# Optimization experiments

Hardware: AMD Instinct MI355X
Metric: run time of the kernel (lower is better)

The kernel has to match this reference:

```python
import jax, jax.numpy as jnp
import numpy as np

N_SURF, N_GRAPH, K_EIG = 30000, 12000, 128
C_IN_SURF, C_IN_GRAPH, C_OUT = 5, 20, 1
HID = 64  # C_width // 2
N_BLOCK = 4
NEIGH_TH = 8.0
BOX = 90.0
E_GRAPH = 192000


def _build_bipartite(rng):
    # exact math of compute_bipartite_graphs: cdist < neigh_th, w = exp(-d/sigma)
    verts = rng.random((N_SURF, 3), dtype=np.float32) * BOX
    pos = rng.random((N_GRAPH, 3), dtype=np.float32) * BOX
    sigma = NEIGH_TH / 2.0
    srcs, dsts, ws = [], [], []
    pn = (pos * pos).sum(-1)
    for s in range(0, N_SURF, 2048):
        ch = verts[s:s + 2048]
        d2 = (ch * ch).sum(-1)[:, None] + pn[None, :] - 2.0 * ch @ pos.T
        d = np.sqrt(np.maximum(d2, 0.0))
        ii, jj = np.where(d < NEIGH_TH)
        srcs.append(ii + s)
        dsts.append(jj + N_SURF)  # graph nodes offset by n_surf
        ws.append(np.exp(-d[ii, jj] / sigma))
    return (np.concatenate(srcs).astype(np.int64),
            np.concatenate(dsts).astype(np.int64),
            np.concatenate(ws).astype(np.float32))


def setup_inputs() -> dict:
    key = jax.random.key(0)
    ks = iter(jax.random.split(key, 64))
    rng = np.random.default_rng(0)
    bi_surf, bi_graph, bi_w = _build_bipartite(rng)

    def rn(shape, scale=0.05):
        return jax.random.normal(next(ks), shape, jnp.float32) * scale

    inp = {
        'x_surf': rn((N_SURF, C_IN_SURF), 1.0),
        'x_graph': rn((N_GRAPH, C_IN_GRAPH), 1.0),
        'mass': jax.random.uniform(next(ks), (N_SURF,), jnp.float32) + 0.1,
        'evals': jnp.sort(jax.random.uniform(next(ks), (K_EIG,), jnp.float32)) * 100.0,
        'evecs': rn((N_SURF, K_EIG), 1.0) / np.sqrt(N_SURF),
        'bi_w': jnp.asarray(bi_w),
        'lin1_w': rn((C_IN_SURF, HID)), 'lin1_b': jnp.zeros((HID,), jnp.float32),
        'lin2_w': rn((C_IN_GRAPH, HID)), 'lin2_b': jnp.zeros((HID,), jnp.float32),
        'diff_time': jax.random.uniform(next(ks), (N_BLOCK, HID), jnp.float32) * 0.1 + 1e-3,
        'mlp_w0': rn((N_BLOCK, 2 * HID, HID)), 'mlp_b0': jnp.zeros((N_BLOCK, HID), jnp.float32),
        'mlp_w1': rn((N_BLOCK, HID, HID)), 'mlp_b1': jnp.zeros((N_BLOCK, HID), jnp.float32),
        'mlp_w2': rn((N_BLOCK, HID, HID)), 'mlp_b2': jnp.zeros((N_BLOCK, HID), jnp.float32),
        'gcn_w1': rn((N_BLOCK, HID, HID)), 'gcn_b1': jnp.zeros((N_BLOCK, HID), jnp.float32),
        'gcn_w2': rn((N_BLOCK, HID, HID)), 'gcn_b2': jnp.zeros((N_BLOCK, HID), jnp.float32),
        'gs_w': rn((N_BLOCK - 1, HID, HID)), 'gs_b': jnp.zeros((N_BLOCK - 1, HID), jnp.float32),
        'gs_w_last': rn((HID, C_OUT)), 'gs_b_last': jnp.zeros((C_OUT,), jnp.float32),
        'sg_w': rn((N_BLOCK - 1, HID, HID)), 'sg_b': jnp.zeros((N_BLOCK - 1, HID), jnp.float32),
        'sg_w_last': rn((HID, C_OUT)), 'sg_b_last': jnp.zeros((C_OUT,), jnp.float32),
        'graph_edge_index': jax.random.randint(next(ks), (2, E_GRAPH), 0, N_GRAPH, jnp.int64),
        'bi_surf': jnp.asarray(bi_surf),
        'bi_graph': jnp.asarray(bi_graph),
    }
    return inp


def gcn_conv(x, W, b, src, dst, ew, n):
    # PyG GCNConv: sym-normalized aggregation with self loops (weight 1)
    h = x @ W
    w = ew if ew is not None else jnp.ones(src.shape, x.dtype)
    deg = jnp.ones((n,), x.dtype).at[dst].add(w)
    dinv = jnp.where(deg > 0, jax.lax.rsqrt(deg), 0.0)
    norm = dinv[src] * dinv[dst] * w
    out = jnp.zeros((n, h.shape[1]), x.dtype).at[dst].add(norm[:, None] * h[src])
    return out + (dinv * dinv)[:, None] * h + b


def reference(x_surf, x_graph, mass, evals, evecs, bi_w,
              lin1_w, lin1_b, lin2_w, lin2_b,
              diff_time, mlp_w0, mlp_b0, mlp_w1, mlp_b1, mlp_w2, mlp_b2,
              gcn_w1, gcn_b1, gcn_w2, gcn_b2,
              gs_w, gs_b, gs_w_last, gs_b_last,
              sg_w, sg_b, sg_w_last, sg_b_last,
              graph_edge_index, bi_surf, bi_graph):
    n_surf, n_graph = x_surf.shape[0], x_graph.shape[0]
    n_tot = n_surf + n_graph
    diff_x = x_surf @ lin1_w + lin1_b            # [Ns, HID]
    g_x = x_graph @ lin2_w + lin2_b              # [Ng, HID]
    gsrc, gdst = graph_edge_index[0], graph_edge_index[1]

    for i in range(N_BLOCK):
        # --- DiffusionNet block (spectral diffusion + MLP + skip) ---
        t = jnp.clip(diff_time[i], 1e-8)
        x_spec = evecs.T @ (mass[:, None] * diff_x)                  # [K, HID]
        x_diffuse = evecs @ (jnp.exp(-evals[:, None] * t[None, :]) * x_spec)
        feat = jnp.concatenate([diff_x, x_diffuse], axis=-1)
        h = jax.nn.relu(feat @ mlp_w0[i] + mlp_b0[i])
        h = jax.nn.relu(h @ mlp_w1[i] + mlp_b1[i])
        h = h @ mlp_w2[i] + mlp_b2[i]
        diff_x = diff_x + h
        # --- internal GCN on molecular graph (use_distance=False) ---
        hg = jax.nn.relu(gcn_conv(g_x, gcn_w1[i], gcn_b1[i], gsrc, gdst, None, n_graph))
        g_x = gcn_conv(hg, gcn_w2[i], gcn_b2[i], gsrc, gdst, None, n_graph)
        # --- bipartite mixing over combined node set ---
        x_cat = jnp.concatenate([diff_x, g_x], axis=0)               # [Ns+Ng, HID]
        if i < N_BLOCK - 1:
            new_surf = gcn_conv(x_cat, gs_w[i], gs_b[i], bi_graph, bi_surf, bi_w, n_tot)[:n_surf]
            new_graph = gcn_conv(x_cat, sg_w[i], sg_b[i], bi_surf, bi_graph, bi_w, n_tot)[n_surf:]
        else:
            new_surf = gcn_conv(x_cat, gs_w_last, gs_b_last, bi_graph, bi_surf, bi_w, n_tot)[:n_surf]
            new_graph = gcn_conv(x_cat, sg_w_last, sg_b_last, bi_surf, bi_graph, bi_w, n_tot)[n_surf:]
        diff_x, g_x = new_surf, new_graph

    return jnp.concatenate([diff_x, g_x], axis=0)  # [Ns+Ng, C_out]
```

## Files before the change

kernel.cpp:

```cpp
#include <hip/hip_runtime.h>

#define N_SURF 30000
#define N_GRAPH 12000
#define K_EIG 128
#define HID 64
#define E_GRAPH 192000

static inline int cdiv(int a, int b) { return (a + b - 1) / b; }

__global__ void k_fill(float* __restrict__ p, float v, int n) {
    int t = blockIdx.x * blockDim.x + threadIdx.x;
    if (t < n) p[t] = v;
}

__global__ void k_filli(int* __restrict__ p, int v, int n) {
    int t = blockIdx.x * blockDim.x + threadIdx.x;
    if (t < n) p[t] = v;
}

__global__ void k_to_dinv(float* __restrict__ p, int n) {
    int t = blockIdx.x * blockDim.x + threadIdx.x;
    if (t < n) p[t] = 1.0f / sqrtf(p[t]);
}

__global__ void k_deg_graph(const int* __restrict__ gdst, float* __restrict__ deg, int E) {
    int t = blockIdx.x * blockDim.x + threadIdx.x;
    if (t < E) atomicAdd(&deg[gdst[t]], 1.0f);
}

__global__ void k_deg_bi(const int* __restrict__ bs, const int* __restrict__ bg,
                         const float* __restrict__ w, float* __restrict__ deg_s,
                         float* __restrict__ deg_g, int E) {
    int t = blockIdx.x * blockDim.x + threadIdx.x;
    if (t < E) {
        float wv = w[t];
        atomicAdd(&deg_s[bs[t]], wv);
        atomicAdd(&deg_g[bg[t] - N_SURF], wv);
    }
}

__global__ void k_hist_bi(const int* __restrict__ bs, const int* __restrict__ bg,
                          int* __restrict__ cnt_s, int* __restrict__ cnt_g, int E) {
    int t = blockIdx.x * blockDim.x + threadIdx.x;
    if (t < E) {
        atomicAdd(&cnt_s[bs[t]], 1);
        atomicAdd(&cnt_g[bg[t] - N_SURF], 1);
    }
}

__global__ void k_hist_gr(const int* __restrict__ gdst, int* __restrict__ cnt, int E) {
    int t = blockIdx.x * blockDim.x + threadIdx.x;
    if (t < E) atomicAdd(&cnt[gdst[t]], 1);
}

__global__ __launch_bounds__(256) void k_scan(const int* __restrict__ cnt,
                                              int* __restrict__ rowptr, int n) {
    __shared__ int part[256];
    int per = (n + 255) / 256;
    int lo = threadIdx.x * per, hi = min(lo + per, n);
    int s = 0;
    for (int i = lo; i < hi; ++i) s += cnt[i];
    part[threadIdx.x] = s;
    __syncthreads();
    for (int off = 1; off < 256; off <<= 1) {
        int v = (threadIdx.x >= off) ? part[threadIdx.x - off] : 0;
        __syncthreads();
        part[threadIdx.x] += v;
        __syncthreads();
    }
    int base = (threadIdx.x == 0) ? 0 : part[threadIdx.x - 1];
    for (int i = lo; i < hi; ++i) { rowptr[i] = base; base += cnt[i]; }
    if (threadIdx.x == 0) rowptr[n] = part[255];
}

__global__ void k_fill_csr_bi(const int* __restrict__ bs, const int* __restrict__ bg,
                              const float* __restrict__ w, const float* __restrict__ dinv_s,
                              const float* __restrict__ dinv_g,
                              const int* __restrict__ rp_s, int* __restrict__ cur_s,
                              int* __restrict__ csr_s_src, float* __restrict__ csr_s_nrm,
                              const int* __restrict__ rp_g, int* __restrict__ cur_g,
                              int* __restrict__ csr_g_src, float* __restrict__ csr_g_nrm,
                              int E) {
    int t = blockIdx.x * blockDim.x + threadIdx.x;
    if (t >= E) return;
    int s = bs[t], g = bg[t] - N_SURF;
    float wv = w[t];
    int ps = rp_s[s] + atomicAdd(&cur_s[s], 1);
    csr_s_src[ps] = g;
    csr_s_nrm[ps] = dinv_s[s] * wv;
    int pg = rp_g[g] + atomicAdd(&cur_g[g], 1);
    csr_g_src[pg] = s;
    csr_g_nrm[pg] = dinv_g[g] * wv;
}

__global__ void k_fill_csr_gr(const int* __restrict__ ei, const float* __restrict__ dinv,
                              const int* __restrict__ rp, int* __restrict__ cur,
                              int* __restrict__ csr_src, float* __restrict__ csr_nrm, int E) {
    int t = blockIdx.x * blockDim.x + threadIdx.x;
    if (t >= E) return;
    int s = ei[t], d = ei[E + t];
    int p = rp[d] + atomicAdd(&cur[d], 1);
    csr_src[p] = s;
    csr_nrm[p] = dinv[s] * dinv[d];
}

__global__ void k_lin(const float* __restrict__ X, const float* __restrict__ W,
                      const float* __restrict__ b, float* __restrict__ out, int M, int K) {
    int t = blockIdx.x * blockDim.x + threadIdx.x;
    if (t >= M * HID) return;
    int r = t >> 6, h = t & 63;
    float acc = b[h];
    for (int k = 0; k < K; ++k) acc = fmaf(X[r * K + k], W[k * HID + h], acc);
    out[t] = acc;
}

__global__ __launch_bounds__(256) void k_spec(const float* __restrict__ evecs,
                                              const float* __restrict__ mass,
                                              const float* __restrict__ dx,
                                              float* __restrict__ spec) {
    __shared__ float evs[32 * 128];
    __shared__ float xms[32 * 64];
    const int h = threadIdx.x & 63, eg = threadIdx.x >> 6;
    float acc[32];
#pragma unroll
    for (int i = 0; i < 32; ++i) acc[i] = 0.f;
    for (int r0 = blockIdx.x * 32; r0 < N_SURF; r0 += gridDim.x * 32) {
        __syncthreads();
        for (int idx = threadIdx.x; idx < 32 * 128; idx += 256) {
            int rr = idx >> 7, k = idx & 127;
            int row = r0 + rr;
            evs[idx] = (row < N_SURF) ? evecs[(size_t)row * 128 + k] : 0.f;
        }
        for (int idx = threadIdx.x; idx < 32 * 64; idx += 256) {
            int rr = idx >> 6, c = idx & 63;
            int row = r0 + rr;
            xms[idx] = (row < N_SURF) ? mass[row] * dx[(size_t)row * 64 + c] : 0.f;
        }
        __syncthreads();
        for (int rr = 0; rr < 32; ++rr) {
            float xv = xms[rr * 64 + h];
            const float* ep = &evs[rr * 128 + eg * 32];
#pragma unroll
            for (int e = 0; e < 32; ++e) acc[e] = fmaf(ep[e], xv, acc[e]);
        }
    }
#pragma unroll
    for (int e = 0; e < 32; ++e) atomicAdd(&spec[(eg * 32 + e) * 64 + h], acc[e]);
}

__global__ void k_bscale(const float* __restrict__ spec, const float* __restrict__ evals,
                         const float* __restrict__ t, float* __restrict__ Bs) {
    int idx = blockIdx.x * blockDim.x + threadIdx.x;
    if (idx >= 128 * 64) return;
    int k = idx >> 6, h = idx & 63;
    float tt = fmaxf(t[h], 1e-8f);
    Bs[idx] = expf(-evals[k] * tt) * spec[idx];
}

template <int K, bool RELU_A>
__global__ __launch_bounds__(256) void k_gemm64(const float* __restrict__ A,
                                                const float* __restrict__ B,
                                                float* __restrict__ C, int M) {
    __shared__ float Bs[K * 64];
    __shared__ float As[64 * K];
    for (int idx = threadIdx.x; idx < K * 64; idx += 256) Bs[idx] = B[idx];
    const int h = threadIdx.x & 63, rg = threadIdx.x >> 6;
    for (int r0 = blockIdx.x * 64; r0 < M; r0 += gridDim.x * 64) {
        __syncthreads();
        for (int idx = threadIdx.x; idx < 64 * K; idx += 256) {
            int rr = idx / K, k = idx - rr * K;
            int row = r0 + rr;
            float v = (row < M) ? A[(size_t)row * K + k] : 0.f;
            if (RELU_A) v = fmaxf(v, 0.f);
            As[idx] = v;
        }
        __syncthreads();
        float acc[16];
#pragma unroll
        for (int i = 0; i < 16; ++i) acc[i] = 0.f;
        for (int k = 0; k < K; k += 4) {
            float b0 = Bs[(k + 0) * 64 + h], b1 = Bs[(k + 1) * 64 + h];
            float b2 = Bs[(k + 2) * 64 + h], b3 = Bs[(k + 3) * 64 + h];
#pragma unroll
            for (int i = 0; i < 16; ++i) {
                const float* ap = &As[(rg * 16 + i) * K + k];
                acc[i] = fmaf(ap[0], b0, fmaf(ap[1], b1, fmaf(ap[2], b2, fmaf(ap[3], b3, acc[i]))));
            }
        }
#pragma unroll
        for (int i = 0; i < 16; ++i) {
            int row = r0 + rg * 16 + i;
            if (row < M) C[(size_t)row * 64 + h] = acc[i];
        }
    }
}

__global__ __launch_bounds__(256) void k_mlp(float* __restrict__ dx, const float* __restrict__ xd,
                                             const float* __restrict__ w0, const float* __restrict__ b0,
                                             const float* __restrict__ w1, const float* __restrict__ b1,
                                             const float* __restrict__ w2, const float* __restrict__ b2,
                                             int M) {
    __shared__ float w0s[128 * 64];
    __shared__ float w1s[64 * 64];
    __shared__ float w2s[64 * 64];
    __shared__ float bsh[3][64];
    __shared__ float feat[4][128];
    __shared__ float h1s[4][64];
    __shared__ float h2s[4][64];
    for (int idx = threadIdx.x; idx < 8192; idx += 256) w0s[idx] = w0[idx];
    for (int idx = threadIdx.x; idx < 4096; idx += 256) { w1s[idx] = w1[idx]; w2s[idx] = w2[idx]; }
    if (threadIdx.x < 64) {
        bsh[0][threadIdx.x] = b0[threadIdx.x];
        bsh[1][threadIdx.x] = b1[threadIdx.x];
        bsh[2][threadIdx.x] = b2[threadIdx.x];
    }
    const int h = threadIdx.x & 63, rg = threadIdx.x >> 6;
    for (int r0 = blockIdx.x * 4; r0 < M; r0 += gridDim.x * 4) {
        int r = r0 + rg;
        __syncthreads();
        feat[rg][h] = dx[(size_t)r * 64 + h];
        feat[rg][64 + h] = xd[(size_t)r * 64 + h];
        __syncthreads();
        float acc = bsh[0][h];
        for (int k = 0; k < 128; k += 4) {
            const float* fp = &feat[rg][k];
            acc = fmaf(fp[0], w0s[(k + 0) * 64 + h],
                  fmaf(fp[1], w0s[(k + 1) * 64 + h],
                  fmaf(fp[2], w0s[(k + 2) * 64 + h],
                  fmaf(fp[3], w0s[(k + 3) * 64 + h], acc))));
        }
        h1s[rg][h] = fmaxf(acc, 0.f);
        __syncthreads();
        acc = bsh[1][h];
        for (int k = 0; k < 64; k += 4) {
            const float* fp = &h1s[rg][k];
            acc = fmaf(fp[0], w1s[(k + 0) * 64 + h],
                  fmaf(fp[1], w1s[(k + 1) * 64 + h],
                  fmaf(fp[2], w1s[(k + 2) * 64 + h],
                  fmaf(fp[3], w1s[(k + 3) * 64 + h], acc))));
        }
        h2s[rg][h] = fmaxf(acc, 0.f);
        __syncthreads();
        acc = bsh[2][h];
        for (int k = 0; k < 64; k += 4) {
            const float* fp = &h2s[rg][k];
            acc = fmaf(fp[0], w2s[(k + 0) * 64 + h],
                  fmaf(fp[1], w2s[(k + 1) * 64 + h],
                  fmaf(fp[2], w2s[(k + 2) * 64 + h],
                  fmaf(fp[3], w2s[(k + 3) * 64 + h], acc))));
        }
        dx[(size_t)r * 64 + h] += acc;
    }
}

__global__ __launch_bounds__(256) void k_gather64(
    const int* __restrict__ rowptr, const int* __restrict__ csr_src,
    const float* __restrict__ csr_nrm, const float* __restrict__ Hsrc,
    const float* __restrict__ Hself, const float* __restrict__ dinv,
    const float* __restrict__ b, float* __restrict__ out, int M) {
    int r = blockIdx.x * 4 + (threadIdx.x >> 6);
    int h = threadIdx.x & 63;
    if (r >= M) return;
    int e0 = rowptr[r], e1 = rowptr[r + 1];
    float dv = dinv[r];
    float acc = fmaf(dv * dv, Hself[(size_t)r * 64 + h], b[h]);
    int e = e0;
    for (; e + 1 < e1; e += 2) {
        float n0 = csr_nrm[e], n1 = csr_nrm[e + 1];
        int s0 = csr_src[e], s1 = csr_src[e + 1];
        acc = fmaf(n0, Hsrc[(size_t)s0 * 64 + h], acc);
        acc = fmaf(n1, Hsrc[(size_t)s1 * 64 + h], acc);
    }
    if (e < e1) acc = fmaf(csr_nrm[e], Hsrc[(size_t)csr_src[e] * 64 + h], acc);
    out[(size_t)r * 64 + h] = acc;
}

__global__ __launch_bounds__(256) void k_gather1(
    const int* __restrict__ rowptr, const int* __restrict__ csr_src,
    const float* __restrict__ csr_nrm, const float* __restrict__ H1src,
    const float* __restrict__ H1self, const float* __restrict__ dinv,
    const float* __restrict__ b, float* __restrict__ out, int M) {
    int r = blockIdx.x * 4 + (threadIdx.x >> 6);
    int l = threadIdx.x & 63;
    if (r >= M) return;
    int e0 = rowptr[r], e1 = rowptr[r + 1];
    float acc = 0.f;
    for (int e = e0 + l; e < e1; e += 64)
        acc = fmaf(csr_nrm[e], H1src[csr_src[e]], acc);
    for (int off = 32; off; off >>= 1) acc += __shfl_down(acc, off, 64);
    if (l == 0) {
        float dv = dinv[r];
        out[r] = fmaf(dv * dv, H1self[r], b[0]) + acc;
    }
}

__global__ void k_gemv64(const float* __restrict__ A, const float* __restrict__ w,
                         float* __restrict__ out, int M) {
    int gid = blockIdx.x * blockDim.x + threadIdx.x;
    int r = gid >> 6, l = gid & 63;
    if (r >= M) return;
    float v = A[(size_t)r * 64 + l] * w[l];
    for (int off = 32; off; off >>= 1) v += __shfl_down(v, off, 64);
    if (l == 0) out[r] = v;
}

extern "C" void kernel_launch(void* const* d_in, const int* in_sizes, int n_in,
                              void* d_out, int out_size, void* d_ws, size_t ws_size,
                              hipStream_t stream) {
    const float* x_surf   = (const float*)d_in[0];
    const float* x_graph  = (const float*)d_in[1];
    const float* mass     = (const float*)d_in[2];
    const float* evals    = (const float*)d_in[3];
    const float* evecs    = (const float*)d_in[4];
    const float* bi_w     = (const float*)d_in[5];
    const float* lin1_w   = (const float*)d_in[6];
    const float* lin1_b   = (const float*)d_in[7];
    const float* lin2_w   = (const float*)d_in[8];
    const float* lin2_b   = (const float*)d_in[9];
    const float* diff_time= (const float*)d_in[10];
    const float* mlp_w0   = (const float*)d_in[11];
    const float* mlp_b0   = (const float*)d_in[12];
    const float* mlp_w1   = (const float*)d_in[13];
    const float* mlp_b1   = (const float*)d_in[14];
    const float* mlp_w2   = (const float*)d_in[15];
    const float* mlp_b2   = (const float*)d_in[16];
    const float* gcn_w1   = (const float*)d_in[17];
    const float* gcn_b1   = (const float*)d_in[18];
    const float* gcn_w2   = (const float*)d_in[19];
    const float* gcn_b2   = (const float*)d_in[20];
    const float* gs_w     = (const float*)d_in[21];
    const float* gs_b     = (const float*)d_in[22];
    const float* gs_w_last= (const float*)d_in[23];
    const float* gs_b_last= (const float*)d_in[24];
    const float* sg_w     = (const float*)d_in[25];
    const float* sg_b     = (const float*)d_in[26];
    const float* sg_w_last= (const float*)d_in[27];
    const float* sg_b_last= (const float*)d_in[28];
    const int* graph_ei   = (const int*)d_in[29];
    const int* bi_s       = (const int*)d_in[30];
    const int* bi_g       = (const int*)d_in[31];
    const int E = in_sizes[5];
    float* out = (float*)d_out;

    float* p = (float*)d_ws;
    float* surfA = p; p += (size_t)N_SURF * 64;
    float* surfB = p; p += (size_t)N_SURF * 64;
    float* xd    = p; p += (size_t)N_SURF * 64;
    float* hs    = p; p += (size_t)N_SURF * 64;
    float* gA    = p; p += (size_t)N_GRAPH * 64;
    float* gB    = p; p += (size_t)N_GRAPH * 64;
    float* tmpg  = p; p += (size_t)N_GRAPH * 64;
    float* hg    = p; p += (size_t)N_GRAPH * 64;
    float* spec  = p; p += 128 * 64;
    float* Bsc   = p; p += 128 * 64;
    float* dinv_s  = p; p += N_SURF;
    float* dinv_g  = p; p += N_GRAPH;
    float* dinv_gr = p; p += N_GRAPH;
    int* cnt_s = (int*)p; p += N_SURF;
    int* cnt_g = (int*)p; p += N_GRAPH;
    int* cnt_gr= (int*)p; p += N_GRAPH;
    int* rp_s  = (int*)p; p += N_SURF + 1;
    int* rp_g  = (int*)p; p += N_GRAPH + 1;
    int* rp_gr = (int*)p; p += N_GRAPH + 1;
    int*   csr_s_src = (int*)p;   p += E;
    float* csr_s_nrm = p;         p += E;
    int*   csr_g_src = (int*)p;   p += E;
    float* csr_g_nrm = p;         p += E;
    int*   csr_gr_src= (int*)p;   p += E_GRAPH;
    float* csr_gr_nrm= p;         p += E_GRAPH;

    float* dx  = surfA;
    float* nsx = surfB;
    float* gx  = gA;
    float* gx2 = gB;

    k_lin<<<cdiv(N_SURF * 64, 256), 256, 0, stream>>>(x_surf, lin1_w, lin1_b, dx, N_SURF, 5);
    k_lin<<<cdiv(N_GRAPH * 64, 256), 256, 0, stream>>>(x_graph, lin2_w, lin2_b, gx, N_GRAPH, 20);
    k_fill<<<cdiv(N_SURF, 256), 256, 0, stream>>>(dinv_s, 1.f, N_SURF);
    k_fill<<<cdiv(N_GRAPH, 256), 256, 0, stream>>>(dinv_g, 1.f, N_GRAPH);
    k_fill<<<cdiv(N_GRAPH, 256), 256, 0, stream>>>(dinv_gr, 1.f, N_GRAPH);
    k_deg_graph<<<cdiv(E_GRAPH, 256), 256, 0, stream>>>(graph_ei + E_GRAPH, dinv_gr, E_GRAPH);
    k_deg_bi<<<cdiv(E, 256), 256, 0, stream>>>(bi_s, bi_g, bi_w, dinv_s, dinv_g, E);
    k_to_dinv<<<cdiv(N_SURF, 256), 256, 0, stream>>>(dinv_s, N_SURF);
    k_to_dinv<<<cdiv(N_GRAPH, 256), 256, 0, stream>>>(dinv_g, N_GRAPH);
    k_to_dinv<<<cdiv(N_GRAPH, 256), 256, 0, stream>>>(dinv_gr, N_GRAPH);
    k_filli<<<cdiv(N_SURF, 256), 256, 0, stream>>>(cnt_s, 0, N_SURF);
    k_filli<<<cdiv(N_GRAPH, 256), 256, 0, stream>>>(cnt_g, 0, N_GRAPH);
    k_filli<<<cdiv(N_GRAPH, 256), 256, 0, stream>>>(cnt_gr, 0, N_GRAPH);
    k_hist_bi<<<cdiv(E, 256), 256, 0, stream>>>(bi_s, bi_g, cnt_s, cnt_g, E);
    k_hist_gr<<<cdiv(E_GRAPH, 256), 256, 0, stream>>>(graph_ei + E_GRAPH, cnt_gr, E_GRAPH);
    k_scan<<<1, 256, 0, stream>>>(cnt_s, rp_s, N_SURF);
    k_scan<<<1, 256, 0, stream>>>(cnt_g, rp_g, N_GRAPH);
    k_scan<<<1, 256, 0, stream>>>(cnt_gr, rp_gr, N_GRAPH);
    k_filli<<<cdiv(N_SURF, 256), 256, 0, stream>>>(cnt_s, 0, N_SURF);
    k_filli<<<cdiv(N_GRAPH, 256), 256, 0, stream>>>(cnt_g, 0, N_GRAPH);
    k_filli<<<cdiv(N_GRAPH, 256), 256, 0, stream>>>(cnt_gr, 0, N_GRAPH);
    k_fill_csr_bi<<<cdiv(E, 256), 256, 0, stream>>>(bi_s, bi_g, bi_w, dinv_s, dinv_g,
                                                    rp_s, cnt_s, csr_s_src, csr_s_nrm,
                                                    rp_g, cnt_g, csr_g_src, csr_g_nrm, E);
    k_fill_csr_gr<<<cdiv(E_GRAPH, 256), 256, 0, stream>>>(graph_ei, dinv_gr, rp_gr, cnt_gr,
                                                          csr_gr_src, csr_gr_nrm, E_GRAPH);

    const int gS = cdiv(N_SURF, 64);
    const int gG = cdiv(N_GRAPH, 64);

    for (int i = 0; i < 4; ++i) {
        k_fill<<<cdiv(128 * 64, 256), 256, 0, stream>>>(spec, 0.f, 128 * 64);
        k_spec<<<240, 256, 0, stream>>>(evecs, mass, dx, spec);
        k_bscale<<<32, 256, 0, stream>>>(spec, evals, diff_time + i * 64, Bsc);
        k_gemm64<128, false><<<gS, 256, 0, stream>>>(evecs, Bsc, xd, N_SURF);
        k_mlp<<<938, 256, 0, stream>>>(dx, xd, mlp_w0 + i * 8192, mlp_b0 + i * 64,
                                       mlp_w1 + i * 4096, mlp_b1 + i * 64,
                                       mlp_w2 + i * 4096, mlp_b2 + i * 64, N_SURF);
        k_gemm64<64, false><<<gG, 256, 0, stream>>>(gx, gcn_w1 + i * 4096, hg, N_GRAPH);
        k_gather64<<<cdiv(N_GRAPH, 4), 256, 0, stream>>>(rp_gr, csr_gr_src, csr_gr_nrm,
                                                         hg, hg, dinv_gr, gcn_b1 + i * 64,
                                                         tmpg, N_GRAPH);
        k_gemm64<64, true><<<gG, 256, 0, stream>>>(tmpg, gcn_w2 + i * 4096, hg, N_GRAPH);
        k_gather64<<<cdiv(N_GRAPH, 4), 256, 0, stream>>>(rp_gr, csr_gr_src, csr_gr_nrm,
                                                         hg, hg, dinv_gr, gcn_b2 + i * 64,
                                                         gx2, N_GRAPH);

        if (i < 3) {
            k_gemm64<64, false><<<gS, 256, 0, stream>>>(dx, gs_w + i * 4096, hs, N_SURF);
            k_gemm64<64, false><<<gG, 256, 0, stream>>>(gx2, gs_w + i * 4096, hg, N_GRAPH);
            k_gather64<<<cdiv(N_SURF, 4), 256, 0, stream>>>(rp_s, csr_s_src, csr_s_nrm,
                                                            hg, hs, dinv_s, gs_b + i * 64,
                                                            nsx, N_SURF);
            k_gemm64<64, false><<<gS, 256, 0, stream>>>(dx, sg_w + i * 4096, hs, N_SURF);
            k_gemm64<64, false><<<gG, 256, 0, stream>>>(gx2, sg_w + i * 4096, hg, N_GRAPH);
            k_gather64<<<cdiv(N_GRAPH, 4), 256, 0, stream>>>(rp_g, csr_g_src, csr_g_nrm,
                                                             hs, hg, dinv_g, sg_b + i * 64,
                                                             gx, N_GRAPH);
            float* t = dx; dx = nsx; nsx = t;
        } else {
            float* hs1 = hs;
            float* hg1 = hs + N_SURF;
            k_gemv64<<<cdiv(N_SURF, 4), 256, 0, stream>>>(dx, gs_w_last, hs1, N_SURF);
            k_gemv64<<<cdiv(N_GRAPH, 4), 256, 0, stream>>>(gx2, gs_w_last, hg1, N_GRAPH);
            k_gather1<<<cdiv(N_SURF, 4), 256, 0, stream>>>(rp_s, csr_s_src, csr_s_nrm,
                                                           hg1, hs1, dinv_s, gs_b_last,
                                                           out, N_SURF);
            k_gemv64<<<cdiv(N_SURF, 4), 256, 0, stream>>>(dx, sg_w_last, hs1, N_SURF);
            k_gemv64<<<cdiv(N_GRAPH, 4), 256, 0, stream>>>(gx2, sg_w_last, hg1, N_GRAPH);
            k_gather1<<<cdiv(N_GRAPH, 4), 256, 0, stream>>>(rp_g, csr_g_src, csr_g_nrm,
                                                            hs1, hg1, dinv_g, sg_b_last,
                                                            out + N_SURF, N_GRAPH);
        }
    }
}
```

Measured before the change: 2.094 ms.

## Pack CSR into int2, merge surf/graph GEMMs, replace spectral atomics with partial reduce

Interleaves CSR source index and normalization into int2 so the gather kernels issue one load per edge. The surface CSR skips its atomic scatter because the bipartite edges are already sorted by surface index. Degree and histogram passes are fused, and paired surface/graph GEMMs and GEMVs are merged into single launches over a concatenated row range. The spectral projection now writes per-block partials that a reduce kernel sums instead of using atomics, and the eigenvector GEMM uses 32-row tiles for more blocks. The sorted-order assumption ties the surface CSR to how the edges are generated, and the partial buffer adds memory traffic.

```diff
diff --git a/kernel.cpp b/kernel.cpp
--- a/kernel.cpp
+++ b/kernel.cpp
@@ -5,6 +5,7 @@
 #define K_EIG 128
 #define HID 64
 #define E_GRAPH 192000
+#define NPART 240
 
 static inline int cdiv(int a, int b) { return (a + b - 1) / b; }
 
@@ -23,34 +24,29 @@
     if (t < n) p[t] = 1.0f / sqrtf(p[t]);
 }
 
-__global__ void k_deg_graph(const int* __restrict__ gdst, float* __restrict__ deg, int E) {
-    int t = blockIdx.x * blockDim.x + threadIdx.x;
-    if (t < E) atomicAdd(&deg[gdst[t]], 1.0f);
-}
-
-__global__ void k_deg_bi(const int* __restrict__ bs, const int* __restrict__ bg,
-                         const float* __restrict__ w, float* __restrict__ deg_s,
-                         float* __restrict__ deg_g, int E) {
+__global__ void k_deg_hist_bi(const int* __restrict__ bs, const int* __restrict__ bg,
+                              const float* __restrict__ w, float* __restrict__ deg_s,
+                              float* __restrict__ deg_g, int* __restrict__ cnt_s,
+                              int* __restrict__ cnt_g, int E) {
     int t = blockIdx.x * blockDim.x + threadIdx.x;
     if (t < E) {
+        int s = bs[t], g = bg[t] - N_SURF;
         float wv = w[t];
-        atomicAdd(&deg_s[bs[t]], wv);
-        atomicAdd(&deg_g[bg[t] - N_SURF], wv);
-    }
-}
-
-__global__ void k_hist_bi(const int* __restrict__ bs, const int* __restrict__ bg,
-                          int* __restrict__ cnt_s, int* __restrict__ cnt_g, int E) {
+        atomicAdd(&deg_s[s], wv);
+        atomicAdd(&deg_g[g], wv);
+        atomicAdd(&cnt_s[s], 1);
+        atomicAdd(&cnt_g[g], 1);
+    }
+}
+
+__global__ void k_deg_hist_gr(const int* __restrict__ gdst, float* __restrict__ deg,
+                              int* __restrict__ cnt, int E) {
     int t = blockIdx.x * blockDim.x + threadIdx.x;
     if (t < E) {
-        atomicAdd(&cnt_s[bs[t]], 1);
-        atomicAdd(&cnt_g[bg[t] - N_SURF], 1);
-    }
-}
-
-__global__ void k_hist_gr(const int* __restrict__ gdst, int* __restrict__ cnt, int E) {
-    int t = blockIdx.x * blockDim.x + threadIdx.x;
-    if (t < E) atomicAdd(&cnt[gdst[t]], 1);
+        int d = gdst[t];
+        atomicAdd(&deg[d], 1.0f);
+        atomicAdd(&cnt[d], 1);
+    }
 }
 
 __global__ __launch_bounds__(256) void k_scan(const int* __restrict__ cnt,
@@ -73,35 +69,34 @@
     if (threadIdx.x == 0) rowptr[n] = part[255];
 }
 
-__global__ void k_fill_csr_bi(const int* __restrict__ bs, const int* __restrict__ bg,
-                              const float* __restrict__ w, const float* __restrict__ dinv_s,
-                              const float* __restrict__ dinv_g,
-                              const int* __restrict__ rp_s, int* __restrict__ cur_s,
-                              int* __restrict__ csr_s_src, float* __restrict__ csr_s_nrm,
-                              const int* __restrict__ rp_g, int* __restrict__ cur_g,
-                              int* __restrict__ csr_g_src, float* __restrict__ csr_g_nrm,
-                              int E) {
+__global__ void k_fill_csr_s_seq(const int* __restrict__ bs, const int* __restrict__ bg,
+                                 const float* __restrict__ w, const float* __restrict__ dinv_s,
+                                 int2* __restrict__ csr, int E) {
     int t = blockIdx.x * blockDim.x + threadIdx.x;
     if (t >= E) return;
     int s = bs[t], g = bg[t] - N_SURF;
-    float wv = w[t];
-    int ps = rp_s[s] + atomicAdd(&cur_s[s], 1);
-    csr_s_src[ps] = g;
-    csr_s_nrm[ps] = dinv_s[s] * wv;
-    int pg = rp_g[g] + atomicAdd(&cur_g[g], 1);
-    csr_g_src[pg] = s;
-    csr_g_nrm[pg] = dinv_g[g] * wv;
+    csr[t] = make_int2(g, __float_as_int(dinv_s[s] * w[t]));
+}
+
+__global__ void k_fill_csr_g(const int* __restrict__ bs, const int* __restrict__ bg,
+                             const float* __restrict__ w, const float* __restrict__ dinv_g,
+                             const int* __restrict__ rp, int* __restrict__ cur,
+                             int2* __restrict__ csr, int E) {
+    int t = blockIdx.x * blockDim.x + threadIdx.x;
+    if (t >= E) return;
+    int s = bs[t], g = bg[t] - N_SURF;
+    int pp = rp[g] + atomicAdd(&cur[g], 1);
+    csr[pp] = make_int2(s, __float_as_int(dinv_g[g] * w[t]));
 }
 
 __global__ void k_fill_csr_gr(const int* __restrict__ ei, const float* __restrict__ dinv,
                               const int* __restrict__ rp, int* __restrict__ cur,
-                              int* __restrict__ csr_src, float* __restrict__ csr_nrm, int E) {
+                              int2* __restrict__ csr, int E) {
     int t = blockIdx.x * blockDim.x + threadIdx.x;
     if (t >= E) return;
     int s = ei[t], d = ei[E + t];
-    int p = rp[d] + atomicAdd(&cur[d], 1);
-    csr_src[p] = s;
-    csr_nrm[p] = dinv[s] * dinv[d];
+    int pp = rp[d] + atomicAdd(&cur[d], 1);
+    csr[pp] = make_int2(s, __float_as_int(dinv[s] * dinv[d]));
 }
 
 __global__ void k_lin(const float* __restrict__ X, const float* __restrict__ W,
@@ -114,10 +109,10 @@
     out[t] = acc;
 }
 
-__global__ __launch_bounds__(256) void k_spec(const float* __restrict__ evecs,
-                                              const float* __restrict__ mass,
-                                              const float* __restrict__ dx,
-                                              float* __restrict__ spec) {
+__global__ __launch_bounds__(256) void k_spec_part(const float* __restrict__ evecs,
+                                                   const float* __restrict__ mass,
+                                                   const float* __restrict__ dx,
+                                                   float* __restrict__ partial) {
     __shared__ float evs[32 * 128];
     __shared__ float xms[32 * 64];
     const int h = threadIdx.x & 63, eg = threadIdx.x >> 6;
@@ -144,21 +139,27 @@
             for (int e = 0; e < 32; ++e) acc[e] = fmaf(ep[e], xv, acc[e]);
         }
     }
-#pragma unroll
-    for (int e = 0; e < 32; ++e) atomicAdd(&spec[(eg * 32 + e) * 64 + h], acc[e]);
-}
-
-__global__ void k_bscale(const float* __restrict__ spec, const float* __restrict__ evals,
-                         const float* __restrict__ t, float* __restrict__ Bs) {
+    float* outp = &partial[(size_t)blockIdx.x * 8192];
+#pragma unroll
+    for (int e = 0; e < 32; ++e) outp[(eg * 32 + e) * 64 + h] = acc[e];
+}
+
+__global__ void k_spec_reduce_bscale(const float* __restrict__ partial,
+                                     const float* __restrict__ evals,
+                                     const float* __restrict__ t,
+                                     float* __restrict__ Bsc) {
     int idx = blockIdx.x * blockDim.x + threadIdx.x;
     if (idx >= 128 * 64) return;
     int k = idx >> 6, h = idx & 63;
+    float s = 0.f;
+    for (int b = 0; b < NPART; ++b) s += partial[(size_t)b * 8192 + idx];
     float tt = fmaxf(t[h], 1e-8f);
-    Bs[idx] = expf(-evals[k] * tt) * spec[idx];
+    Bsc[idx] = expf(-evals[k] * tt) * s;
 }
 
 template <int K, bool RELU_A>
-__global__ __launch_bounds__(256) void k_gemm64(const float* __restrict__ A,
+__global__ __launch_bounds__(256) void k_gemm64(const float* __restrict__ A1,
+                                                const float* __restrict__ A2, int M1,
                                                 const float* __restrict__ B,
                                                 float* __restrict__ C, int M) {
     __shared__ float Bs[K * 64];
@@ -170,8 +171,12 @@
         for (int idx = threadIdx.x; idx < 64 * K; idx += 256) {
             int rr = idx / K, k = idx - rr * K;
             int row = r0 + rr;
-            float v = (row < M) ? A[(size_t)row * K + k] : 0.f;
-            if (RELU_A) v = fmaxf(v, 0.f);
+            float v = 0.f;
+            if (row < M) {
+                v = (row < M1) ? A1[(size_t)row * K + k]
+                               : A2[(size_t)(row - M1) * K + k];
+                if (RELU_A) v = fmaxf(v, 0.f);
+            }
             As[idx] = v;
         }
         __syncthreads();
@@ -190,6 +195,41 @@
 #pragma unroll
         for (int i = 0; i < 16; ++i) {
             int row = r0 + rg * 16 + i;
+            if (row < M) C[(size_t)row * 64 + h] = acc[i];
+        }
+    }
+}
+
+__global__ __launch_bounds__(256) void k_gemm128_r32(const float* __restrict__ A,
+                                                     const float* __restrict__ B,
+                                                     float* __restrict__ C, int M) {
+    __shared__ float Bs[128 * 64];
+    __shared__ float As[32 * 128];
+    for (int idx = threadIdx.x; idx < 128 * 64; idx += 256) Bs[idx] = B[idx];
+    const int h = threadIdx.x & 63, rg = threadIdx.x >> 6;
+    for (int r0 = blockIdx.x * 32; r0 < M; r0 += gridDim.x * 32) {
+        __syncthreads();
+        for (int idx = threadIdx.x; idx < 32 * 128; idx += 256) {
+            int rr = idx >> 7, k = idx & 127;
+            int row = r0 + rr;
+            As[idx] = (row < M) ? A[(size_t)row * 128 + k] : 0.f;
+        }
+        __syncthreads();
+        float acc[8];
+#pragma unroll
+        for (int i = 0; i < 8; ++i) acc[i] = 0.f;
+        for (int k = 0; k < 128; k += 4) {
+            float b0 = Bs[(k + 0) * 64 + h], b1 = Bs[(k + 1) * 64 + h];
+            float b2 = Bs[(k + 2) * 64 + h], b3 = Bs[(k + 3) * 64 + h];
+#pragma unroll
+            for (int i = 0; i < 8; ++i) {
+                const float* ap = &As[(rg * 8 + i) * 128 + k];
+                acc[i] = fmaf(ap[0], b0, fmaf(ap[1], b1, fmaf(ap[2], b2, fmaf(ap[3], b3, acc[i]))));
+            }
+        }
+#pragma unroll
+        for (int i = 0; i < 8; ++i) {
+            int row = r0 + rg * 8 + i;
             if (row < M) C[(size_t)row * 64 + h] = acc[i];
         }
     }
@@ -254,10 +294,10 @@
 }
 
 __global__ __launch_bounds__(256) void k_gather64(
-    const int* __restrict__ rowptr, const int* __restrict__ csr_src,
-    const float* __restrict__ csr_nrm, const float* __restrict__ Hsrc,
-    const float* __restrict__ Hself, const float* __restrict__ dinv,
-    const float* __restrict__ b, float* __restrict__ out, int M) {
+    const int* __restrict__ rowptr, const int2* __restrict__ csr,
+    const float* __restrict__ Hsrc, const float* __restrict__ Hself,
+    const float* __restrict__ dinv, const float* __restrict__ b,
+    float* __restrict__ out, int M) {
     int r = blockIdx.x * 4 + (threadIdx.x >> 6);
     int h = threadIdx.x & 63;
     if (r >= M) return;
@@ -266,27 +306,31 @@
     float acc = fmaf(dv * dv, Hself[(size_t)r * 64 + h], b[h]);
     int e = e0;
     for (; e + 1 < e1; e += 2) {
-        float n0 = csr_nrm[e], n1 = csr_nrm[e + 1];
-        int s0 = csr_src[e], s1 = csr_src[e + 1];
-        acc = fmaf(n0, Hsrc[(size_t)s0 * 64 + h], acc);
-        acc = fmaf(n1, Hsrc[(size_t)s1 * 64 + h], acc);
-    }
-    if (e < e1) acc = fmaf(csr_nrm[e], Hsrc[(size_t)csr_src[e] * 64 + h], acc);
+        int2 c0 = csr[e], c1 = csr[e + 1];
+        acc = fmaf(__int_as_float(c0.y), Hsrc[(size_t)c0.x * 64 + h], acc);
+        acc = fmaf(__int_as_float(c1.y), Hsrc[(size_t)c1.x * 64 + h], acc);
+    }
+    if (e < e1) {
+        int2 c = csr[e];
+        acc = fmaf(__int_as_float(c.y), Hsrc[(size_t)c.x * 64 + h], acc);
+    }
     out[(size_t)r * 64 + h] = acc;
 }
 
 __global__ __launch_bounds__(256) void k_gather1(
-    const int* __restrict__ rowptr, const int* __restrict__ csr_src,
-    const float* __restrict__ csr_nrm, const float* __restrict__ H1src,
-    const float* __restrict__ H1self, const float* __restrict__ dinv,
-    const float* __restrict__ b, float* __restrict__ out, int M) {
+    const int* __restrict__ rowptr, const int2* __restrict__ csr,
+    const float* __restrict__ H1src, const float* __restrict__ H1self,
+    const float* __restrict__ dinv, const float* __restrict__ b,
+    float* __restrict__ out, int M) {
     int r = blockIdx.x * 4 + (threadIdx.x >> 6);
     int l = threadIdx.x & 63;
     if (r >= M) return;
     int e0 = rowptr[r], e1 = rowptr[r + 1];
     float acc = 0.f;
-    for (int e = e0 + l; e < e1; e += 64)
-        acc = fmaf(csr_nrm[e], H1src[csr_src[e]], acc);
+    for (int e = e0 + l; e < e1; e += 64) {
+        int2 c = csr[e];
+        acc = fmaf(__int_as_float(c.y), H1src[c.x], acc);
+    }
     for (int off = 32; off; off >>= 1) acc += __shfl_down(acc, off, 64);
     if (l == 0) {
         float dv = dinv[r];
@@ -294,12 +338,13 @@
     }
 }
 
-__global__ void k_gemv64(const float* __restrict__ A, const float* __restrict__ w,
-                         float* __restrict__ out, int M) {
+__global__ void k_gemv64c(const float* __restrict__ A1, const float* __restrict__ A2, int M1,
+                          const float* __restrict__ w, float* __restrict__ out, int M) {
     int gid = blockIdx.x * blockDim.x + threadIdx.x;
     int r = gid >> 6, l = gid & 63;
     if (r >= M) return;
-    float v = A[(size_t)r * 64 + l] * w[l];
+    const float* row = (r < M1) ? &A1[(size_t)r * 64] : &A2[(size_t)(r - M1) * 64];
+    float v = row[l] * w[l];
     for (int off = 32; off; off >>= 1) v += __shfl_down(v, off, 64);
     if (l == 0) out[r] = v;
 }
@@ -346,12 +391,12 @@
     float* surfA = p; p += (size_t)N_SURF * 64;
     float* surfB = p; p += (size_t)N_SURF * 64;
     float* xd    = p; p += (size_t)N_SURF * 64;
-    float* hs    = p; p += (size_t)N_SURF * 64;
+    float* hcat  = p; p += (size_t)(N_SURF + N_GRAPH) * 64;
     float* gA    = p; p += (size_t)N_GRAPH * 64;
     float* gB    = p; p += (size_t)N_GRAPH * 64;
     float* tmpg  = p; p += (size_t)N_GRAPH * 64;
     float* hg    = p; p += (size_t)N_GRAPH * 64;
-    float* spec  = p; p += 128 * 64;
+    float* partial = p; p += (size_t)NPART * 8192;
     float* Bsc   = p; p += 128 * 64;
     float* dinv_s  = p; p += N_SURF;
     float* dinv_g  = p; p += N_GRAPH;
@@ -362,13 +407,12 @@
     int* rp_s  = (int*)p; p += N_SURF + 1;
     int* rp_g  = (int*)p; p += N_GRAPH + 1;
     int* rp_gr = (int*)p; p += N_GRAPH + 1;
-    int*   csr_s_src = (int*)p;   p += E;
-    float* csr_s_nrm = p;         p += E;
-    int*   csr_g_src = (int*)p;   p += E;
-    float* csr_g_nrm = p;         p += E;
-    int*   csr_gr_src= (int*)p;   p += E_GRAPH;
-    float* csr_gr_nrm= p;         p += E_GRAPH;
-
+    p += ((size_t)p & 4) ? 1 : 0;
+    int2* csr_s  = (int2*)p; p += 2 * (size_t)E;
+    int2* csr_g  = (int2*)p; p += 2 * (size_t)E;
+    int2* csr_gr = (int2*)p; p += 2 * (size_t)E_GRAPH;
+
+    float* hg_part = hcat + (size_t)N_SURF * 64;
     float* dx  = surfA;
     float* nsx = surfB;
     float* gx  = gA;
@@ -379,73 +423,63 @@
     k_fill<<<cdiv(N_SURF, 256), 256, 0, stream>>>(dinv_s, 1.f, N_SURF);
     k_fill<<<cdiv(N_GRAPH, 256), 256, 0, stream>>>(dinv_g, 1.f, N_GRAPH);
     k_fill<<<cdiv(N_GRAPH, 256), 256, 0, stream>>>(dinv_gr, 1.f, N_GRAPH);
-    k_deg_graph<<<cdiv(E_GRAPH, 256), 256, 0, stream>>>(graph_ei + E_GRAPH, dinv_gr, E_GRAPH);
-    k_deg_bi<<<cdiv(E, 256), 256, 0, stream>>>(bi_s, bi_g, bi_w, dinv_s, dinv_g, E);
+    k_filli<<<cdiv(N_SURF, 256), 256, 0, stream>>>(cnt_s, 0, N_SURF);
+    k_filli<<<cdiv(N_GRAPH, 256), 256, 0, stream>>>(cnt_g, 0, N_GRAPH);
+    k_filli<<<cdiv(N_GRAPH, 256), 256, 0, stream>>>(cnt_gr, 0, N_GRAPH);
+    k_deg_hist_bi<<<cdiv(E, 256), 256, 0, stream>>>(bi_s, bi_g, bi_w, dinv_s, dinv_g,
+                                                    cnt_s, cnt_g, E);
+    k_deg_hist_gr<<<cdiv(E_GRAPH, 256), 256, 0, stream>>>(graph_ei + E_GRAPH, dinv_gr, cnt_gr, E_GRAPH);
     k_to_dinv<<<cdiv(N_SURF, 256), 256, 0, stream>>>(dinv_s, N_SURF);
     k_to_dinv<<<cdiv(N_GRAPH, 256), 256, 0, stream>>>(dinv_g, N_GRAPH);
     k_to_dinv<<<cdiv(N_GRAPH, 256), 256, 0, stream>>>(dinv_gr, N_GRAPH);
-    k_filli<<<cdiv(N_SURF, 256), 256, 0, stream>>>(cnt_s, 0, N_SURF);
-    k_filli<<<cdiv(N_GRAPH, 256), 256, 0, stream>>>(cnt_g, 0, N_GRAPH);
-    k_filli<<<cdiv(N_GRAPH, 256), 256, 0, stream>>>(cnt_gr, 0, N_GRAPH);
-    k_hist_bi<<<cdiv(E, 256), 256, 0, stream>>>(bi_s, bi_g, cnt_s, cnt_g, E);
-    k_hist_gr<<<cdiv(E_GRAPH, 256), 256, 0, stream>>>(graph_ei + E_GRAPH, cnt_gr, E_GRAPH);
     k_scan<<<1, 256, 0, stream>>>(cnt_s, rp_s, N_SURF);
     k_scan<<<1, 256, 0, stream>>>(cnt_g, rp_g, N_GRAPH);
     k_scan<<<1, 256, 0, stream>>>(cnt_gr, rp_gr, N_GRAPH);
-    k_filli<<<cdiv(N_SURF, 256), 256, 0, stream>>>(cnt_s, 0, N_SURF);
+    k_fill_csr_s_seq<<<cdiv(E, 256), 256, 0, stream>>>(bi_s, bi_g, bi_w, dinv_s, csr_s, E);
     k_filli<<<cdiv(N_GRAPH, 256), 256, 0, stream>>>(cnt_g, 0, N_GRAPH);
     k_filli<<<cdiv(N_GRAPH, 256), 256, 0, stream>>>(cnt_gr, 0, N_GRAPH);
-    k_fill_csr_bi<<<cdiv(E, 256), 256, 0, stream>>>(bi_s, bi_g, bi_w, dinv_s, dinv_g,
-                                                    rp_s, cnt_s, csr_s_src, csr_s_nrm,
-                                                    rp_g, cnt_g, csr_g_src, csr_g_nrm, E);
+    k_fill_csr_g<<<cdiv(E, 256), 256, 0, stream>>>(bi_s, bi_g, bi_w, dinv_g, rp_g, cnt_g, csr_g, E);
     k_fill_csr_gr<<<cdiv(E_GRAPH, 256), 256, 0, stream>>>(graph_ei, dinv_gr, rp_gr, cnt_gr,
-                                                          csr_gr_src, csr_gr_nrm, E_GRAPH);
-
-    const int gS = cdiv(N_SURF, 64);
+                                                          csr_gr, E_GRAPH);
+
     const int gG = cdiv(N_GRAPH, 64);
+    const int gC = cdiv(N_SURF + N_GRAPH, 64);
 
     for (int i = 0; i < 4; ++i) {
-        k_fill<<<cdiv(128 * 64, 256), 256, 0, stream>>>(spec, 0.f, 128 * 64);
-        k_spec<<<240, 256, 0, stream>>>(evecs, mass, dx, spec);
-        k_bscale<<<32, 256, 0, stream>>>(spec, evals, diff_time + i * 64, Bsc);
-        k_gemm64<128, false><<<gS, 256, 0, stream>>>(evecs, Bsc, xd, N_SURF);
+        k_spec_part<<<NPART, 256, 0, stream>>>(evecs, mass, dx, partial);
+        k_spec_reduce_bscale<<<32, 256, 0, stream>>>(partial, evals, diff_time + i * 64, Bsc);
+        k_gemm128_r32<<<938, 256, 0, stream>>>(evecs, Bsc, xd, N_SURF);
         k_mlp<<<938, 256, 0, stream>>>(dx, xd, mlp_w0 + i * 8192, mlp_b0 + i * 64,
                                        mlp_w1 + i * 4096, mlp_b1 + i * 64,
                                        mlp_w2 + i * 4096, mlp_b2 + i * 64, N_SURF);
-        k_gemm64<64, false><<<gG, 256, 0, stream>>>(gx, gcn_w1 + i * 4096, hg, N_GRAPH);
-        k_gather64<<<cdiv(N_GRAPH, 4), 256, 0, stream>>>(rp_gr, csr_gr_src, csr_gr_nrm,
-                                                         hg, hg, dinv_gr, gcn_b1 + i * 64,
-                                                         tmpg, N_GRAPH);
-        k_gemm64<64, true><<<gG, 256, 0, stream>>>(tmpg, gcn_w2 + i * 4096, hg, N_GRAPH);
-        k_gather64<<<cdiv(N_GRAPH, 4), 256, 0, stream>>>(rp_gr, csr_gr_src, csr_gr_nrm,
-                                                         hg, hg, dinv_gr, gcn_b2 + i * 64,
-                                                         gx2, N_GRAPH);
+        k_gemm64<64, false><<<gG, 256, 0, stream>>>(gx, gx, N_GRAPH, gcn_w1 + i * 4096, hg, N_GRAPH);
+        k_gather64<<<cdiv(N_GRAPH, 4), 256, 0, stream>>>(rp_gr, csr_gr, hg, hg, dinv_gr,
+                                                         gcn_b1 + i * 64, tmpg, N_GRAPH);
+        k_gemm64<64, true><<<gG, 256, 0, stream>>>(tmpg, tmpg, N_GRAPH, gcn_w2 + i * 4096, hg, N_GRAPH);
+        k_gather64<<<cdiv(N_GRAPH, 4), 256, 0, stream>>>(rp_gr, csr_gr, hg, hg, dinv_gr,
+                                                         gcn_b2 + i * 64, gx2, N_GRAPH);
 
         if (i < 3) {
-            k_gemm64<64, false><<<gS, 256, 0, stream>>>(dx, gs_w + i * 4096, hs, N_SURF);
-            k_gemm64<64, false><<<gG, 256, 0, stream>>>(gx2, gs_w + i * 4096, hg, N_GRAPH);
-            k_gather64<<<cdiv(N_SURF, 4), 256, 0, stream>>>(rp_s, csr_s_src, csr_s_nrm,
-                                                            hg, hs, dinv_s, gs_b + i * 64,
-                                                            nsx, N_SURF);
-            k_gemm64<64, false><<<gS, 256, 0, stream>>>(dx, sg_w + i * 4096, hs, N_SURF);
-            k_gemm64<64, false><<<gG, 256, 0, stream>>>(gx2, sg_w + i * 4096, hg, N_GRAPH);
-            k_gather64<<<cdiv(N_GRAPH, 4), 256, 0, stream>>>(rp_g, csr_g_src, csr_g_nrm,
-                                                             hs, hg, dinv_g, sg_b + i * 64,
-                                                             gx, N_GRAPH);
+            k_gemm64<64, false><<<gC, 256, 0, stream>>>(dx, gx2, N_SURF, gs_w + i * 4096,
+                                                        hcat, N_SURF + N_GRAPH);
+            k_gather64<<<cdiv(N_SURF, 4), 256, 0, stream>>>(rp_s, csr_s, hg_part, hcat, dinv_s,
+                                                            gs_b + i * 64, nsx, N_SURF);
+            k_gemm64<64, false><<<gC, 256, 0, stream>>>(dx, gx2, N_SURF, sg_w + i * 4096,
+                                                        hcat, N_SURF + N_GRAPH);
+            k_gather64<<<cdiv(N_GRAPH, 4), 256, 0, stream>>>(rp_g, csr_g, hcat, hg_part, dinv_g,
+                                                             sg_b + i * 64, gx, N_GRAPH);
             float* t = dx; dx = nsx; nsx = t;
         } else {
-            float* hs1 = hs;
-            float* hg1 = hs + N_SURF;
-            k_gemv64<<<cdiv(N_SURF, 4), 256, 0, stream>>>(dx, gs_w_last, hs1, N_SURF);
-            k_gemv64<<<cdiv(N_GRAPH, 4), 256, 0, stream>>>(gx2, gs_w_last, hg1, N_GRAPH);
-            k_gather1<<<cdiv(N_SURF, 4), 256, 0, stream>>>(rp_s, csr_s_src, csr_s_nrm,
-                                                           hg1, hs1, dinv_s, gs_b_last,
-                                                           out, N_SURF);
-            k_gemv64<<<cdiv(N_SURF, 4), 256, 0, stream>>>(dx, sg_w_last, hs1, N_SURF);
-            k_gemv64<<<cdiv(N_GRAPH, 4), 256, 0, stream>>>(gx2, sg_w_last, hg1, N_GRAPH);
-            k_gather1<<<cdiv(N_GRAPH, 4), 256, 0, stream>>>(rp_g, csr_g_src, csr_g_nrm,
-                                                            hs1, hg1, dinv_g, sg_b_last,
-                                                            out + N_SURF, N_GRAPH);
-        }
-    }
-}
+            float* h1 = hcat;
+            float* h1g = hcat + N_SURF;
+            k_gemv64c<<<cdiv((N_SURF + N_GRAPH) * 64, 256), 256, 0, stream>>>(
+                dx, gx2, N_SURF, gs_w_last, h1, N_SURF + N_GRAPH);
+            k_gather1<<<cdiv(N_SURF, 4), 256, 0, stream>>>(rp_s, csr_s, h1g, h1, dinv_s,
+                                                           gs_b_last, out, N_SURF);
+            k_gemv64c<<<cdiv((N_SURF + N_GRAPH) * 64, 256), 256, 0, stream>>>(
+                dx, gx2, N_SURF, sg_w_last, h1, N_SURF + N_GRAPH);
+            k_gather1<<<cdiv(N_GRAPH, 4), 256, 0, stream>>>(rp_g, csr_g, h1, h1g, dinv_g,
+                                                            sg_b_last, out + N_SURF, N_GRAPH);
+        }
+    }
+}
```

After: 1.827 ms. 1.15x faster.
